# Performance work log

Hardware: AMD Instinct MI355X
Metric: run time of the kernel (lower is better)

Reference implementation:

```python
import jax, jax.numpy as jnp
import numpy as np

NUM_HEADS = 16
NEG_INF = -1e30


def setup_inputs() -> dict:
    key = jax.random.key(0)
    k1, k2, k3 = jax.random.split(key, 3)
    B, S, D = 2, 2048, 1024
    x = jax.random.normal(k1, (B, S, D), dtype=jnp.float32)
    # torch Linear(D, 3D, bias=False) stored here already transposed: y = x @ w_qkv
    w_qkv = jax.random.normal(k2, (D, 3 * D), dtype=jnp.float32) * 0.02
    w_out = jax.random.normal(k3, (D, D), dtype=jnp.float32) * 0.02
    return {"x": x, "w_qkv": w_qkv, "w_out": w_out}


def reference(x, w_qkv, w_out):
    B, S, D = x.shape
    H = NUM_HEADS
    dh = D // H
    qkv = x @ w_qkv                      # [B, S, 3D]
    q, k, v = jnp.split(qkv, 3, axis=-1)

    def to_heads(t):
        return t.reshape(B, S, H, dh).transpose(0, 2, 1, 3)  # [B, H, S, dh]

    q, k, v = to_heads(q), to_heads(k), to_heads(v)
    scale = jnp.asarray(dh, x.dtype) ** -0.5
    scores = jnp.einsum('bhqd,bhkd->bhqk', q, k) * scale     # [B, H, S, S]
    causal = jnp.tril(jnp.ones((S, S), dtype=bool))
    scores = jnp.where(causal, scores, NEG_INF)
    attn = jax.nn.softmax(scores, axis=-1)
    out = jnp.einsum('bhqk,bhkd->bhqd', attn, v)             # [B, H, S, dh]
    out = out.transpose(0, 2, 1, 3).reshape(B, S, D)
    return out @ w_out
```

## Files before the change

kernel.cpp:

```cpp
#include <hip/hip_runtime.h>

typedef unsigned short u16;
typedef unsigned int u32;

typedef __bf16 bf16x8 __attribute__((ext_vector_type(8)));
typedef _Float16 f16x8 __attribute__((ext_vector_type(8)));
typedef float f32x4 __attribute__((ext_vector_type(4)));

typedef __attribute__((address_space(1))) u32 as1_u32;
typedef __attribute__((address_space(3))) u32 as3_u32;

#define EKF 0.18033688011112042f

__device__ __forceinline__ u16 f2bf(float x) {
  u32 u = __float_as_uint(x);
  u = u + 0x7fffu + ((u >> 16) & 1u);
  return (u16)(u >> 16);
}
__device__ __forceinline__ u32 pack2(float a, float b) {
  return (u32)f2bf(a) | ((u32)f2bf(b) << 16);
}
__device__ __forceinline__ u32 pkf16(float a, float b) {
  return __builtin_bit_cast(u32, __builtin_amdgcn_cvt_pkrtz(a, b));
}
__device__ __forceinline__ u16 f2h(float a) {
  return (u16)(pkf16(a, a) & 0xffffu);
}
__device__ __forceinline__ void gld_lds16(const u16* g, const u16* l) {
  __builtin_amdgcn_global_load_lds((const as1_u32*)g, (as3_u32*)l, 16, 0, 0);
}

__global__ __launch_bounds__(256) void prepass_kernel(const float* __restrict__ x,
                                                      const float* __restrict__ w_qkv,
                                                      const float* __restrict__ w_out,
                                                      u16* __restrict__ xb,
                                                      u16* __restrict__ wqkvT,
                                                      u16* __restrict__ woutT) {
  __shared__ float tile[64][65];
  int bid = blockIdx.x;
  int t = threadIdx.x;
  if (bid < 4096) {
    int i = bid * 256 + t;
    float4 v = ((const float4*)x)[i];
    uint2 r;
    r.x = pack2(v.x, v.y);
    r.y = pack2(v.z, v.w);
    ((uint2*)xb)[i] = r;
    return;
  }
  const float* W;
  u16* WT;
  int K, N, bx, by;
  if (bid < 4096 + 768) {
    int b2 = bid - 4096;
    W = w_qkv; WT = wqkvT; K = 1024; N = 3072; bx = b2 & 15; by = b2 >> 4;
  } else {
    int b2 = bid - 4864;
    W = w_out; WT = woutT; K = 1024; N = 1024; bx = b2 & 15; by = b2 >> 4;
  }
  int k0 = bx * 64, n0 = by * 64;
  int r = t >> 4, c4 = (t & 15) * 4;
#pragma unroll
  for (int i = 0; i < 4; ++i) {
    int row = r + i * 16;
    float4 v = *(const float4*)&W[(size_t)(k0 + row) * N + n0 + c4];
    tile[row][c4 + 0] = v.x; tile[row][c4 + 1] = v.y;
    tile[row][c4 + 2] = v.z; tile[row][c4 + 3] = v.w;
  }
  __syncthreads();
#pragma unroll
  for (int i = 0; i < 4; ++i) {
    int n = r + i * 16;
    uint2 o;
    o.x = pack2(tile[c4 + 0][n], tile[c4 + 1][n]);
    o.y = pack2(tile[c4 + 2][n], tile[c4 + 3][n]);
    *(uint2*)&WT[(size_t)(n0 + n) * K + k0 + c4] = o;
  }
}

__global__ __launch_bounds__(512, 2) void gemm_qkv256_kernel(const u16* __restrict__ A,
                                                             const u16* __restrict__ BT,
                                                             u16* __restrict__ QK,
                                                             u16* __restrict__ VT) {
  __shared__ __attribute__((aligned(16))) u16 smem[65536];
  const int tid = threadIdx.x;
  const int wave = tid >> 6;
  const int lane = tid & 63;
  const int lr = lane & 15;
  const int kg = lane >> 4;
  const int l7 = lr & 7;
  const int wr = wave >> 2;
  const int wc = wave & 3;

  int b = blockIdx.x;
  int sw = (b & 7) * 24 + (b >> 3);
  const int bn = (sw % 12) * 256;
  const int bm = (sw / 12) * 256;

  const int srow = tid >> 3;
  const int scg = ((tid & 7) ^ (srow & 7)) * 8;
  const u16* pa = A + (size_t)(bm + srow) * 1024 + scg;
  const u16* pb = BT + (size_t)(bn + srow) * 1024 + scg;
  const u32 lw = (u32)wave * 512;

  f32x4 acc[8][4];
#pragma unroll
  for (int i = 0; i < 8; ++i)
#pragma unroll
    for (int j = 0; j < 4; ++j) {
      f32x4 z = {0.f, 0.f, 0.f, 0.f};
      acc[i][j] = z;
    }

  {
    u16* dA = (u16*)smem;
    u16* dB = (u16*)smem + 16384;
#pragma unroll
    for (int i = 0; i < 4; ++i) gld_lds16(pa + (size_t)(i * 64) * 1024, dA + lw + i * 4096);
#pragma unroll
    for (int i = 0; i < 4; ++i) gld_lds16(pb + (size_t)(i * 64) * 1024, dB + lw + i * 4096);
  }

  for (int t = 0; t < 16; ++t) {
    __syncthreads();
    const u16* bA = smem + (t & 1) * 32768;
    const u16* bB = bA + 16384;
    if (t + 1 < 16) {
      u16* dA = (u16*)smem + ((t + 1) & 1) * 32768;
      u16* dB = dA + 16384;
      const int k1 = (t + 1) * 64;
#pragma unroll
      for (int i = 0; i < 4; ++i) gld_lds16(pa + (size_t)(i * 64) * 1024 + k1, dA + lw + i * 4096);
#pragma unroll
      for (int i = 0; i < 4; ++i) gld_lds16(pb + (size_t)(i * 64) * 1024 + k1, dB + lw + i * 4096);
    }
    bf16x8 bfr[2][4];
#pragma unroll
    for (int kh = 0; kh < 2; ++kh)
#pragma unroll
      for (int ni = 0; ni < 4; ++ni)
        bfr[kh][ni] = *(const bf16x8*)(bB + (wc * 64 + ni * 16 + lr) * 64 +
                                       (((kh * 4 + kg) ^ l7) * 8));
#pragma unroll
    for (int ph = 0; ph < 4; ++ph) {
      const int mh = ph >> 1, kh = ph & 1;
      bf16x8 af[4];
#pragma unroll
      for (int mi = 0; mi < 4; ++mi)
        af[mi] = *(const bf16x8*)(bA + (wr * 128 + mh * 64 + mi * 16 + lr) * 64 +
                                  (((kh * 4 + kg) ^ l7) * 8));
      __builtin_amdgcn_s_barrier();
      __builtin_amdgcn_s_setprio(1);
#pragma unroll
      for (int mi = 0; mi < 4; ++mi)
#pragma unroll
        for (int ni = 0; ni < 4; ++ni)
          acc[mh * 4 + mi][ni] = __builtin_amdgcn_mfma_f32_16x16x32_bf16(
              bfr[kh][ni], af[mi], acc[mh * 4 + mi][ni], 0, 0, 0);
      __builtin_amdgcn_s_setprio(0);
      __builtin_amdgcn_s_barrier();
    }
  }

  __syncthreads();
  if (bn >= 2048) {
#pragma unroll
    for (int mi = 0; mi < 8; ++mi)
#pragma unroll
      for (int ni = 0; ni < 4; ++ni) {
        int r = bm + wr * 128 + mi * 16 + lr;
        int c = bn + wc * 64 + ni * 16 + kg * 4 - 2048;
        int bh2 = (r >> 11) * 16 + (c >> 6);
        int j = r & 2047;
        u16* vrow = VT + ((size_t)bh2 * 64 + (c & 63)) * 2048 + j;
        f32x4 a = acc[mi][ni];
#pragma unroll
        for (int rr = 0; rr < 4; ++rr) vrow[(size_t)rr * 2048] = f2h(a[rr]);
      }
  } else {
    float scale = (bn < 1024) ? EKF : 1.0f;
#pragma unroll
    for (int mi = 0; mi < 8; ++mi)
#pragma unroll
      for (int ni = 0; ni < 4; ++ni) {
        int row = wr * 128 + mi * 16 + lr;
        u32 off = (u32)row * 256 + wc * 64 + (((ni * 4 + kg) ^ (lr & 6)) * 4);
        f32x4 a = acc[mi][ni];
        *(uint2*)((u16*)smem + off) =
            make_uint2(pack2(a[0] * scale, a[1] * scale), pack2(a[2] * scale, a[3] * scale));
      }
    __syncthreads();
#pragma unroll
    for (int i = 0; i < 16; ++i) {
      int row = i * 16 + (tid >> 5);
      int lc = tid & 31;
      int blk = lc >> 3, cc = lc & 7;
      uint4 v = *(const uint4*)((const u16*)smem + (u32)row * 256 + blk * 64 +
                                (((2 * cc) ^ (row & 6)) * 4));
      *(uint4*)(QK + (size_t)(bm + row) * 2048 + bn + blk * 64 + cc * 8) = v;
    }
  }
}

__global__ __launch_bounds__(256, 2) void gemm_out_kernel(const u16* __restrict__ A,
                                                          const u16* __restrict__ BT,
                                                          float* __restrict__ C) {
  __shared__ __attribute__((aligned(16))) u16 smem[2][12288];
  const int tid = threadIdx.x;
  const int wave = tid >> 6;
  const int lane = tid & 63;
  const int lr = lane & 15;
  const int kg = lane >> 4;
  const int lr7 = lr & 7;
  const int wm = (wave >> 1) * 32;
  const int wn = (wave & 1) * 64;

  const int b = blockIdx.x;
  const int xcd = b & 7, loc = b >> 3;
  const int bm = (xcd * 8 + (loc >> 3)) * 64;
  const int bn = (loc & 7) * 128;

  const int sr = tid >> 3;
  const int scg = ((tid & 7) ^ (sr & 7)) * 8;
  const u16* pa = A + (size_t)(bm + sr) * 1024 + scg;
  const u16* pb = BT + (size_t)(bn + sr) * 1024 + scg;
  const u32 lw = (u32)wave * 512;

  f32x4 acc[2][4];
#pragma unroll
  for (int i = 0; i < 2; ++i)
#pragma unroll
    for (int j = 0; j < 4; ++j) {
      f32x4 z = {0.f, 0.f, 0.f, 0.f};
      acc[i][j] = z;
    }

  {
    u16* dA = smem[0];
    u16* dB = smem[0] + 4096;
#pragma unroll
    for (int i = 0; i < 2; ++i) gld_lds16(pa + (size_t)(i * 32) * 1024, dA + lw + i * 2048);
#pragma unroll
    for (int i = 0; i < 4; ++i) gld_lds16(pb + (size_t)(i * 32) * 1024, dB + lw + i * 2048);
  }

  for (int t = 0; t < 16; ++t) {
    __syncthreads();
    const u16* bA = smem[t & 1];
    const u16* bB = bA + 4096;
    if (t + 1 < 16) {
      u16* dA = smem[(t + 1) & 1];
      u16* dB = dA + 4096;
      const int k1 = (t + 1) * 64;
#pragma unroll
      for (int i = 0; i < 2; ++i) gld_lds16(pa + (size_t)(i * 32) * 1024 + k1, dA + lw + i * 2048);
#pragma unroll
      for (int i = 0; i < 4; ++i) gld_lds16(pb + (size_t)(i * 32) * 1024 + k1, dB + lw + i * 2048);
    }
#pragma unroll
    for (int kk = 0; kk < 2; ++kk) {
      const int ch = ((kk * 4 + kg) ^ lr7) * 8;
      bf16x8 af[2], bfr[4];
#pragma unroll
      for (int mi = 0; mi < 2; ++mi)
        af[mi] = *(const bf16x8*)(bA + (wm + mi * 16 + lr) * 64 + ch);
#pragma unroll
      for (int ni = 0; ni < 4; ++ni)
        bfr[ni] = *(const bf16x8*)(bB + (wn + ni * 16 + lr) * 64 + ch);
      __builtin_amdgcn_s_setprio(1);
#pragma unroll
      for (int mi = 0; mi < 2; ++mi)
#pragma unroll
        for (int ni = 0; ni < 4; ++ni)
          acc[mi][ni] = __builtin_amdgcn_mfma_f32_16x16x32_bf16(bfr[ni], af[mi], acc[mi][ni], 0, 0, 0);
      __builtin_amdgcn_s_setprio(0);
    }
  }

  float* buf = (float*)smem;
#pragma unroll
  for (int hc = 0; hc < 2; ++hc) {
    __syncthreads();
    if ((wave & 1) == hc) {
#pragma unroll
      for (int mi = 0; mi < 2; ++mi)
#pragma unroll
        for (int ni = 0; ni < 4; ++ni) {
          int row = wm + mi * 16 + lr;
          int cp = ((ni * 4 + kg) ^ lr) * 4;
          *(f32x4*)(buf + row * 64 + cp) = acc[mi][ni];
        }
    }
    __syncthreads();
#pragma unroll
    for (int i = 0; i < 4; ++i) {
      int row = i * 16 + (tid >> 4);
      int lc = tid & 15;
      float4 v = *(const float4*)(buf + row * 64 + ((lc ^ (row & 15)) * 4));
      *(float4*)(C + (size_t)(bm + row) * 1024 + bn + hc * 64 + lc * 4) = v;
    }
  }
}

__global__ __launch_bounds__(256, 4) void attn_mfma_kernel(const u16* __restrict__ qk,
                                                           const u16* __restrict__ vt,
                                                           u16* __restrict__ out) {
  __shared__ __attribute__((aligned(16))) u16 sK[2][64 * 64];
  __shared__ __attribute__((aligned(16))) u16 sV[2][64 * 64];
  __shared__ __attribute__((aligned(16))) u16 sP[4][16 * 64];

  const int tid = threadIdx.x;
  const int wave = tid >> 6;
  const int lane = tid & 63;
  const int lr = lane & 15;
  const int kg = lane >> 4;
  const int l7 = lr & 7;

  int idx = blockIdx.x;
  int qi = 31 - (idx >> 5);
  int bh = (idx & 7) * 4 + ((idx >> 3) & 3);
  int b = bh >> 4, h = bh & 15;
  int q0 = qi * 64;

  const u16* qbase = qk + (size_t)b * 2048 * 2048 + h * 64;
  const u16* kbase = qbase + 1024;
  const u16* vbase = vt + (size_t)bh * 64 * 2048;
  u16* obase = out + (size_t)b * 2048 * 1024 + h * 64;

  const int sra = wave * 16 + (lane >> 3);
  const int srb = sra + 8;
  const int sc = lane & 7;
  const u32 koffA = (u32)sra * 2048 + (u32)((sc ^ (sra & 7)) * 8);
  const u32 koffB = (u32)srb * 2048 + (u32)((sc ^ (srb & 7)) * 8);
  const u32 ldsA = (wave * 2 + 0) * 512;
  const u32 ldsB = (wave * 2 + 1) * 512;

  const int qcol = q0 + wave * 16 + lr;
  bf16x8 qf0, qf1;
  {
    const u16* qrow = qbase + (size_t)qcol * 2048;
    qf0 = *(const bf16x8*)(qrow + kg * 8);
    qf1 = *(const bf16x8*)(qrow + 32 + kg * 8);
  }

  const u32 ka0 = (u32)(lr * 64 + ((kg ^ l7) * 8));
  const u32 ka1 = (u32)(lr * 64 + (((4 + kg) ^ l7) * 8));
  u16* const sPw = sP[wave];
  const u32 pr0 = (u32)(lr * 64 + (((kg * 2) ^ (l7 << 1)) * 4));
  const u32 pr1 = (u32)(lr * 64 + (((8 + kg * 2) ^ (l7 << 1)) * 4));

  f32x4 oacc[4];
#pragma unroll
  for (int i = 0; i < 4; ++i) {
    f32x4 z = {0.f, 0.f, 0.f, 0.f};
    oacc[i] = z;
  }
  float lsum = 0.f;

  const int nrounds = qi + 1;
  gld_lds16(kbase + koffA, sK[0] + ldsA);
  gld_lds16(kbase + koffB, sK[0] + ldsB);
  gld_lds16(vbase + koffA, sV[0] + ldsA);
  gld_lds16(vbase + koffB, sV[0] + ldsB);
  __syncthreads();

  for (int t = 0; t < nrounds; ++t) {
    if (t + 1 < nrounds) {
      int j1 = (t + 1) * 64;
      u16* dK = sK[(t + 1) & 1];
      u16* dV = sV[(t + 1) & 1];
      gld_lds16(kbase + (size_t)j1 * 2048 + koffA, dK + ldsA);
      gld_lds16(kbase + (size_t)j1 * 2048 + koffB, dK + ldsB);
      gld_lds16(vbase + j1 + koffA, dV + ldsA);
      gld_lds16(vbase + j1 + koffB, dV + ldsB);
    }
    const u16* sKb = sK[t & 1];
    const u16* sVb = sV[t & 1];
    const bool diag = (t == qi);

#pragma unroll
    for (int jt = 0; jt < 4; ++jt) {
      u16* pw = sPw + lr * 64 + (((jt * 4 + kg) ^ (l7 << 1)) * 4);
      if (!diag || jt <= wave) {
        bf16x8 kf0 = *(const bf16x8*)(sKb + jt * 1024 + ka0);
        bf16x8 kf1 = *(const bf16x8*)(sKb + jt * 1024 + ka1);
        f32x4 c = {0.f, 0.f, 0.f, 0.f};
        c = __builtin_amdgcn_mfma_f32_16x16x32_bf16(kf0, qf0, c, 0, 0, 0);
        c = __builtin_amdgcn_mfma_f32_16x16x32_bf16(kf1, qf1, c, 0, 0, 0);
        float p0 = exp2f(c[0]);
        float p1 = exp2f(c[1]);
        float p2 = exp2f(c[2]);
        float p3 = exp2f(c[3]);
        if (diag && jt == wave) {
          int jr = kg * 4;
          p0 = (jr + 0 <= lr) ? p0 : 0.f;
          p1 = (jr + 1 <= lr) ? p1 : 0.f;
          p2 = (jr + 2 <= lr) ? p2 : 0.f;
          p3 = (jr + 3 <= lr) ? p3 : 0.f;
        }
        lsum += (p0 + p1) + (p2 + p3);
        *(uint2*)pw = make_uint2(pkf16(p0, p1), pkf16(p2, p3));
      } else {
        *(uint2*)pw = make_uint2(0u, 0u);
      }
    }

    asm volatile("" ::: "memory");

    f16x8 pf0 = *(const f16x8*)(sPw + pr0);
    f16x8 pf1 = *(const f16x8*)(sPw + pr1);
    __builtin_amdgcn_s_setprio(1);
#pragma unroll
    for (int dt = 0; dt < 4; ++dt) {
      f16x8 vf0 = *(const f16x8*)(sVb + dt * 1024 + ka0);
      f16x8 vf1 = *(const f16x8*)(sVb + dt * 1024 + ka1);
      oacc[dt] = __builtin_amdgcn_mfma_f32_16x16x32_f16(vf0, pf0, oacc[dt], 0, 0, 0);
      oacc[dt] = __builtin_amdgcn_mfma_f32_16x16x32_f16(vf1, pf1, oacc[dt], 0, 0, 0);
    }
    __builtin_amdgcn_s_setprio(0);
    __syncthreads();
  }

  lsum += __shfl_xor(lsum, 16);
  lsum += __shfl_xor(lsum, 32);
  float inv = 1.0f / lsum;

  u16* orow = obase + (size_t)qcol * 1024;
#pragma unroll
  for (int dt = 0; dt < 4; ++dt) {
    uint2 o2 = make_uint2(pack2(oacc[dt][0] * inv, oacc[dt][1] * inv),
                          pack2(oacc[dt][2] * inv, oacc[dt][3] * inv));
    *(uint2*)(orow + dt * 16 + kg * 4) = o2;
  }
}

extern "C" void kernel_launch(void* const* d_in, const int* in_sizes, int n_in,
                              void* d_out, int out_size, void* d_ws, size_t ws_size,
                              hipStream_t stream) {
  const float* x = (const float*)d_in[0];
  const float* w_qkv = (const float*)d_in[1];
  const float* w_out = (const float*)d_in[2];
  float* out = (float*)d_out;

  char* ws = (char*)d_ws;
  u16* xb    = (u16*)(ws);
  u16* wqkvT = (u16*)(ws + (8u << 20));
  u16* woutT = (u16*)(ws + (14u << 20));
  u16* qkb   = (u16*)(ws + (16u << 20));
  u16* vtb   = (u16*)(ws + (32u << 20));
  u16* attn  = (u16*)(ws + (40u << 20));

  prepass_kernel<<<5120, 256, 0, stream>>>(x, w_qkv, w_out, xb, wqkvT, woutT);

  gemm_qkv256_kernel<<<192, 512, 0, stream>>>(xb, wqkvT, qkb, vtb);

  attn_mfma_kernel<<<1024, 256, 0, stream>>>(qkb, vtb, attn);

  gemm_out_kernel<<<512, 256, 0, stream>>>(attn, woutT, out);
}
```

Measured before the change: 163.1 us.

## Split attention waves into 2x2 query/key grid with LDS partial-sum reduction

Changes the wave decomposition in the attention kernel. Each wave used to own 16 query rows across all 64 keys; now each wave owns 32 query rows and 32 keys. Each K and V fragment loaded from LDS is therefore reused across two query subtiles, which roughly halves LDS fragment reads per MFMA. The cost is a final cross-wave reduction of partial outputs and row sums through shared memory, plus an extra barrier and more accumulator registers.

```diff
diff --git a/kernel.cpp b/kernel.cpp
--- a/kernel.cpp
+++ b/kernel.cpp
@@ -307,7 +307,7 @@
                                                            u16* __restrict__ out) {
   __shared__ __attribute__((aligned(16))) u16 sK[2][64 * 64];
   __shared__ __attribute__((aligned(16))) u16 sV[2][64 * 64];
-  __shared__ __attribute__((aligned(16))) u16 sP[4][16 * 64];
+  __shared__ __attribute__((aligned(16))) u16 sP[4][32 * 32];
 
   const int tid = threadIdx.x;
   const int wave = tid >> 6;
@@ -315,6 +315,8 @@
   const int lr = lane & 15;
   const int kg = lane >> 4;
   const int l7 = lr & 7;
+  const int qh = wave & 1;
+  const int jh = wave >> 1;
 
   int idx = blockIdx.x;
   int qi = 31 - (idx >> 5);
@@ -335,27 +337,30 @@
   const u32 ldsA = (wave * 2 + 0) * 512;
   const u32 ldsB = (wave * 2 + 1) * 512;
 
-  const int qcol = q0 + wave * 16 + lr;
-  bf16x8 qf0, qf1;
-  {
-    const u16* qrow = qbase + (size_t)qcol * 2048;
-    qf0 = *(const bf16x8*)(qrow + kg * 8);
-    qf1 = *(const bf16x8*)(qrow + 32 + kg * 8);
+  bf16x8 qf[2][2];
+#pragma unroll
+  for (int qs = 0; qs < 2; ++qs) {
+    const u16* qrow = qbase + (size_t)(q0 + qh * 32 + qs * 16 + lr) * 2048;
+    qf[qs][0] = *(const bf16x8*)(qrow + kg * 8);
+    qf[qs][1] = *(const bf16x8*)(qrow + 32 + kg * 8);
   }
 
   const u32 ka0 = (u32)(lr * 64 + ((kg ^ l7) * 8));
   const u32 ka1 = (u32)(lr * 64 + (((4 + kg) ^ l7) * 8));
+  const u32 kav = jh ? ka1 : ka0;
   u16* const sPw = sP[wave];
-  const u32 pr0 = (u32)(lr * 64 + (((kg * 2) ^ (l7 << 1)) * 4));
-  const u32 pr1 = (u32)(lr * 64 + (((8 + kg * 2) ^ (l7 << 1)) * 4));
-
-  f32x4 oacc[4];
-#pragma unroll
-  for (int i = 0; i < 4; ++i) {
-    f32x4 z = {0.f, 0.f, 0.f, 0.f};
-    oacc[i] = z;
-  }
-  float lsum = 0.f;
+  const u32 pkey = (u32)((lr & 3) << 1);
+  const u32 prd = (u32)(((2 * kg) ^ pkey) * 4);
+
+  f32x4 oacc[2][4];
+#pragma unroll
+  for (int qs = 0; qs < 2; ++qs)
+#pragma unroll
+    for (int dt = 0; dt < 4; ++dt) {
+      f32x4 z = {0.f, 0.f, 0.f, 0.f};
+      oacc[qs][dt] = z;
+    }
+  float ls[2] = {0.f, 0.f};
 
   const int nrounds = qi + 1;
   gld_lds16(kbase + koffA, sK[0] + ldsA);
@@ -379,58 +384,86 @@
     const bool diag = (t == qi);
 
 #pragma unroll
-    for (int jt = 0; jt < 4; ++jt) {
-      u16* pw = sPw + lr * 64 + (((jt * 4 + kg) ^ (l7 << 1)) * 4);
-      if (!diag || jt <= wave) {
-        bf16x8 kf0 = *(const bf16x8*)(sKb + jt * 1024 + ka0);
-        bf16x8 kf1 = *(const bf16x8*)(sKb + jt * 1024 + ka1);
-        f32x4 c = {0.f, 0.f, 0.f, 0.f};
-        c = __builtin_amdgcn_mfma_f32_16x16x32_bf16(kf0, qf0, c, 0, 0, 0);
-        c = __builtin_amdgcn_mfma_f32_16x16x32_bf16(kf1, qf1, c, 0, 0, 0);
-        float p0 = exp2f(c[0]);
-        float p1 = exp2f(c[1]);
-        float p2 = exp2f(c[2]);
-        float p3 = exp2f(c[3]);
-        if (diag && jt == wave) {
-          int jr = kg * 4;
-          p0 = (jr + 0 <= lr) ? p0 : 0.f;
-          p1 = (jr + 1 <= lr) ? p1 : 0.f;
-          p2 = (jr + 2 <= lr) ? p2 : 0.f;
-          p3 = (jr + 3 <= lr) ? p3 : 0.f;
+    for (int jtl = 0; jtl < 2; ++jtl) {
+      const int jtg = jh * 2 + jtl;
+      bf16x8 kf0 = *(const bf16x8*)(sKb + jtg * 1024 + ka0);
+      bf16x8 kf1 = *(const bf16x8*)(sKb + jtg * 1024 + ka1);
+#pragma unroll
+      for (int qs = 0; qs < 2; ++qs) {
+        const int qmin = qh * 32 + qs * 16;
+        u16* pw = sPw + (qs * 16 + lr) * 32 + (((jtl * 4 + kg) ^ pkey) * 4);
+        if (!diag || jtg * 16 <= qmin + 15) {
+          f32x4 c = {0.f, 0.f, 0.f, 0.f};
+          c = __builtin_amdgcn_mfma_f32_16x16x32_bf16(kf0, qf[qs][0], c, 0, 0, 0);
+          c = __builtin_amdgcn_mfma_f32_16x16x32_bf16(kf1, qf[qs][1], c, 0, 0, 0);
+          float p0 = exp2f(c[0]);
+          float p1 = exp2f(c[1]);
+          float p2 = exp2f(c[2]);
+          float p3 = exp2f(c[3]);
+          if (diag && jtg * 16 + 15 > qmin) {
+            int jr = jtg * 16 + kg * 4 - qmin;
+            p0 = (jr + 0 <= lr) ? p0 : 0.f;
+            p1 = (jr + 1 <= lr) ? p1 : 0.f;
+            p2 = (jr + 2 <= lr) ? p2 : 0.f;
+            p3 = (jr + 3 <= lr) ? p3 : 0.f;
+          }
+          ls[qs] += (p0 + p1) + (p2 + p3);
+          *(uint2*)pw = make_uint2(pkf16(p0, p1), pkf16(p2, p3));
+        } else {
+          *(uint2*)pw = make_uint2(0u, 0u);
         }
-        lsum += (p0 + p1) + (p2 + p3);
-        *(uint2*)pw = make_uint2(pkf16(p0, p1), pkf16(p2, p3));
-      } else {
-        *(uint2*)pw = make_uint2(0u, 0u);
       }
     }
 
     asm volatile("" ::: "memory");
 
-    f16x8 pf0 = *(const f16x8*)(sPw + pr0);
-    f16x8 pf1 = *(const f16x8*)(sPw + pr1);
+    f16x8 pf0 = *(const f16x8*)(sPw + (0 * 16 + lr) * 32 + prd);
+    f16x8 pf1 = *(const f16x8*)(sPw + (1 * 16 + lr) * 32 + prd);
     __builtin_amdgcn_s_setprio(1);
 #pragma unroll
     for (int dt = 0; dt < 4; ++dt) {
-      f16x8 vf0 = *(const f16x8*)(sVb + dt * 1024 + ka0);
-      f16x8 vf1 = *(const f16x8*)(sVb + dt * 1024 + ka1);
-      oacc[dt] = __builtin_amdgcn_mfma_f32_16x16x32_f16(vf0, pf0, oacc[dt], 0, 0, 0);
-      oacc[dt] = __builtin_amdgcn_mfma_f32_16x16x32_f16(vf1, pf1, oacc[dt], 0, 0, 0);
+      f16x8 vf = *(const f16x8*)(sVb + dt * 1024 + kav);
+      oacc[0][dt] = __builtin_amdgcn_mfma_f32_16x16x32_f16(vf, pf0, oacc[0][dt], 0, 0, 0);
+      oacc[1][dt] = __builtin_amdgcn_mfma_f32_16x16x32_f16(vf, pf1, oacc[1][dt], 0, 0, 0);
     }
     __builtin_amdgcn_s_setprio(0);
     __syncthreads();
   }
 
-  lsum += __shfl_xor(lsum, 16);
-  lsum += __shfl_xor(lsum, 32);
-  float inv = 1.0f / lsum;
-
-  u16* orow = obase + (size_t)qcol * 1024;
-#pragma unroll
-  for (int dt = 0; dt < 4; ++dt) {
-    uint2 o2 = make_uint2(pack2(oacc[dt][0] * inv, oacc[dt][1] * inv),
-                          pack2(oacc[dt][2] * inv, oacc[dt][3] * inv));
-    *(uint2*)(orow + dt * 16 + kg * 4) = o2;
+  ls[0] += __shfl_xor(ls[0], 16);
+  ls[0] += __shfl_xor(ls[0], 32);
+  ls[1] += __shfl_xor(ls[1], 16);
+  ls[1] += __shfl_xor(ls[1], 32);
+
+  float* obuf = (float*)sK;
+  float* lbuf = (float*)sV;
+  if (jh == 1) {
+#pragma unroll
+    for (int qs = 0; qs < 2; ++qs) {
+      int q = qh * 32 + qs * 16 + lr;
+#pragma unroll
+      for (int dt = 0; dt < 4; ++dt)
+        *(f32x4*)(obuf + q * 64 + (((dt * 4 + kg) ^ l7) * 4)) = oacc[qs][dt];
+      if (kg == 0) lbuf[q] = ls[qs];
+    }
+  }
+  __syncthreads();
+  if (jh == 0) {
+#pragma unroll
+    for (int qs = 0; qs < 2; ++qs) {
+      int q = qh * 32 + qs * 16 + lr;
+      float inv = 1.0f / (ls[qs] + lbuf[q]);
+      u16* orow = obase + (size_t)(q0 + q) * 1024;
+#pragma unroll
+      for (int dt = 0; dt < 4; ++dt) {
+        f32x4 po = *(const f32x4*)(obuf + q * 64 + (((dt * 4 + kg) ^ l7) * 4));
+        float o0 = (oacc[qs][dt][0] + po[0]) * inv;
+        float o1 = (oacc[qs][dt][1] + po[1]) * inv;
+        float o2 = (oacc[qs][dt][2] + po[2]) * inv;
+        float o3 = (oacc[qs][dt][3] + po[3]) * inv;
+        *(uint2*)(orow + dt * 16 + kg * 4) = make_uint2(pack2(o0, o1), pack2(o2, o3));
+      }
+    }
   }
 }
 
```

Result: no change. 165.6 us (+1.5%).

## Switch attention to 32x32 MFMA with register-resident P via permlane swap

Applied to the files above, without the earlier changes.

Reworks the attention inner loop to use 32x32x16 MFMA tiles: waves split queries into two 32-row halves and keys into two 32-column halves. Probabilities are repacked in registers with v_permlane32_swap instead of round-tripping through shared memory, so the sP buffer goes away. Partial outputs and row sums from the two key halves are combined through LDS at the end. This trades fewer LDS writes/reads and fewer MFMA issues for an extra final reduction and coarser causal masking, since the diagonal tile now computes masked work across whole 32-wide blocks.

```diff
diff --git a/kernel.cpp b/kernel.cpp
--- a/kernel.cpp
+++ b/kernel.cpp
@@ -6,6 +6,8 @@
 typedef __bf16 bf16x8 __attribute__((ext_vector_type(8)));
 typedef _Float16 f16x8 __attribute__((ext_vector_type(8)));
 typedef float f32x4 __attribute__((ext_vector_type(4)));
+typedef float f32x16 __attribute__((ext_vector_type(16)));
+typedef u32 u32x4 __attribute__((ext_vector_type(4)));
 
 typedef __attribute__((address_space(1))) u32 as1_u32;
 typedef __attribute__((address_space(3))) u32 as3_u32;
@@ -307,14 +309,14 @@
                                                            u16* __restrict__ out) {
   __shared__ __attribute__((aligned(16))) u16 sK[2][64 * 64];
   __shared__ __attribute__((aligned(16))) u16 sV[2][64 * 64];
-  __shared__ __attribute__((aligned(16))) u16 sP[4][16 * 64];
 
   const int tid = threadIdx.x;
   const int wave = tid >> 6;
   const int lane = tid & 63;
-  const int lr = lane & 15;
-  const int kg = lane >> 4;
-  const int l7 = lr & 7;
+  const int l31 = lane & 31;
+  const int hi = lane >> 5;
+  const int qh = wave & 1;
+  const int jh = wave >> 1;
 
   int idx = blockIdx.x;
   int qi = 31 - (idx >> 5);
@@ -335,27 +337,18 @@
   const u32 ldsA = (wave * 2 + 0) * 512;
   const u32 ldsB = (wave * 2 + 1) * 512;
 
-  const int qcol = q0 + wave * 16 + lr;
-  bf16x8 qf0, qf1;
+  const int qcol = q0 + qh * 32 + l31;
+  bf16x8 qf[4];
   {
     const u16* qrow = qbase + (size_t)qcol * 2048;
-    qf0 = *(const bf16x8*)(qrow + kg * 8);
-    qf1 = *(const bf16x8*)(qrow + 32 + kg * 8);
-  }
-
-  const u32 ka0 = (u32)(lr * 64 + ((kg ^ l7) * 8));
-  const u32 ka1 = (u32)(lr * 64 + (((4 + kg) ^ l7) * 8));
-  u16* const sPw = sP[wave];
-  const u32 pr0 = (u32)(lr * 64 + (((kg * 2) ^ (l7 << 1)) * 4));
-  const u32 pr1 = (u32)(lr * 64 + (((8 + kg * 2) ^ (l7 << 1)) * 4));
-
-  f32x4 oacc[4];
-#pragma unroll
-  for (int i = 0; i < 4; ++i) {
-    f32x4 z = {0.f, 0.f, 0.f, 0.f};
-    oacc[i] = z;
-  }
-  float lsum = 0.f;
+#pragma unroll
+    for (int s = 0; s < 4; ++s) qf[s] = *(const bf16x8*)(qrow + s * 16 + hi * 8);
+  }
+
+  f32x16 oacc[2];
+#pragma unroll
+  for (int i = 0; i < 16; ++i) { oacc[0][i] = 0.f; oacc[1][i] = 0.f; }
+  float ls = 0.f;
 
   const int nrounds = qi + 1;
   gld_lds16(kbase + koffA, sK[0] + ldsA);
@@ -378,59 +371,92 @@
     const u16* sVb = sV[t & 1];
     const bool diag = (t == qi);
 
-#pragma unroll
-    for (int jt = 0; jt < 4; ++jt) {
-      u16* pw = sPw + lr * 64 + (((jt * 4 + kg) ^ (l7 << 1)) * 4);
-      if (!diag || jt <= wave) {
-        bf16x8 kf0 = *(const bf16x8*)(sKb + jt * 1024 + ka0);
-        bf16x8 kf1 = *(const bf16x8*)(sKb + jt * 1024 + ka1);
-        f32x4 c = {0.f, 0.f, 0.f, 0.f};
-        c = __builtin_amdgcn_mfma_f32_16x16x32_bf16(kf0, qf0, c, 0, 0, 0);
-        c = __builtin_amdgcn_mfma_f32_16x16x32_bf16(kf1, qf1, c, 0, 0, 0);
-        float p0 = exp2f(c[0]);
-        float p1 = exp2f(c[1]);
-        float p2 = exp2f(c[2]);
-        float p3 = exp2f(c[3]);
-        if (diag && jt == wave) {
-          int jr = kg * 4;
-          p0 = (jr + 0 <= lr) ? p0 : 0.f;
-          p1 = (jr + 1 <= lr) ? p1 : 0.f;
-          p2 = (jr + 2 <= lr) ? p2 : 0.f;
-          p3 = (jr + 3 <= lr) ? p3 : 0.f;
-        }
-        lsum += (p0 + p1) + (p2 + p3);
-        *(uint2*)pw = make_uint2(pkf16(p0, p1), pkf16(p2, p3));
-      } else {
-        *(uint2*)pw = make_uint2(0u, 0u);
+    f32x16 c;
+#pragma unroll
+    for (int i = 0; i < 16; ++i) c[i] = 0.f;
+#pragma unroll
+    for (int s = 0; s < 4; ++s) {
+      const u32 row = (u32)(jh * 32 + l31);
+      bf16x8 kf = *(const bf16x8*)(sKb + row * 64 + (((2 * s + hi) ^ (row & 7)) * 8));
+      c = __builtin_amdgcn_mfma_f32_32x32x16_bf16(kf, qf[s], c, 0, 0, 0);
+    }
+    float p[16];
+    const int qrel = qh * 32 + l31;
+#pragma unroll
+    for (int r = 0; r < 16; ++r) {
+      int joff = jh * 32 + (r & 3) + 8 * (r >> 2) + 4 * hi;
+      float e = exp2f(c[r]);
+      p[r] = (!diag || (joff <= qrel)) ? e : 0.f;
+    }
+    {
+      float s0 = (p[0] + p[1]) + (p[2] + p[3]);
+      float s1 = (p[4] + p[5]) + (p[6] + p[7]);
+      float s2 = (p[8] + p[9]) + (p[10] + p[11]);
+      float s3 = (p[12] + p[13]) + (p[14] + p[15]);
+      ls += (s0 + s1) + (s2 + s3);
+    }
+    u32 c01 = pkf16(p[0], p[1]),   c23 = pkf16(p[2], p[3]);
+    u32 c45 = pkf16(p[4], p[5]),   c67 = pkf16(p[6], p[7]);
+    u32 c89 = pkf16(p[8], p[9]),   cab = pkf16(p[10], p[11]);
+    u32 ccd = pkf16(p[12], p[13]), cef = pkf16(p[14], p[15]);
+    asm volatile("v_permlane32_swap_b32 %0, %1" : "+v"(c01), "+v"(c45));
+    asm volatile("v_permlane32_swap_b32 %0, %1" : "+v"(c23), "+v"(c67));
+    asm volatile("v_permlane32_swap_b32 %0, %1" : "+v"(c89), "+v"(ccd));
+    asm volatile("v_permlane32_swap_b32 %0, %1" : "+v"(cab), "+v"(cef));
+    u32x4 w0 = {c01, c23, c45, c67};
+    u32x4 w1 = {c89, cab, ccd, cef};
+    f16x8 pa0 = __builtin_bit_cast(f16x8, w0);
+    f16x8 pa1 = __builtin_bit_cast(f16x8, w1);
+
+    __builtin_amdgcn_s_setprio(1);
+#pragma unroll
+    for (int dh = 0; dh < 2; ++dh) {
+      const u32 row = (u32)(dh * 32 + l31);
+#pragma unroll
+      for (int s2 = 0; s2 < 2; ++s2) {
+        f16x8 vf = *(const f16x8*)(sVb + row * 64 +
+                                   (((4 * jh + 2 * s2 + hi) ^ (row & 7)) * 8));
+        oacc[dh] = __builtin_amdgcn_mfma_f32_32x32x16_f16(
+            vf, (s2 == 0) ? pa0 : pa1, oacc[dh], 0, 0, 0);
       }
     }
-
-    asm volatile("" ::: "memory");
-
-    f16x8 pf0 = *(const f16x8*)(sPw + pr0);
-    f16x8 pf1 = *(const f16x8*)(sPw + pr1);
-    __builtin_amdgcn_s_setprio(1);
-#pragma unroll
-    for (int dt = 0; dt < 4; ++dt) {
-      f16x8 vf0 = *(const f16x8*)(sVb + dt * 1024 + ka0);
-      f16x8 vf1 = *(const f16x8*)(sVb + dt * 1024 + ka1);
-      oacc[dt] = __builtin_amdgcn_mfma_f32_16x16x32_f16(vf0, pf0, oacc[dt], 0, 0, 0);
-      oacc[dt] = __builtin_amdgcn_mfma_f32_16x16x32_f16(vf1, pf1, oacc[dt], 0, 0, 0);
-    }
     __builtin_amdgcn_s_setprio(0);
     __syncthreads();
   }
 
-  lsum += __shfl_xor(lsum, 16);
-  lsum += __shfl_xor(lsum, 32);
-  float inv = 1.0f / lsum;
-
-  u16* orow = obase + (size_t)qcol * 1024;
-#pragma unroll
-  for (int dt = 0; dt < 4; ++dt) {
-    uint2 o2 = make_uint2(pack2(oacc[dt][0] * inv, oacc[dt][1] * inv),
-                          pack2(oacc[dt][2] * inv, oacc[dt][3] * inv));
-    *(uint2*)(orow + dt * 16 + kg * 4) = o2;
+  ls += __shfl_xor(ls, 32);
+
+  float* obuf = (float*)sK;
+  float* lbuf = (float*)sV;
+  const int q = qh * 32 + l31;
+  if (jh == 1) {
+#pragma unroll
+    for (int dh = 0; dh < 2; ++dh)
+#pragma unroll
+      for (int g = 0; g < 4; ++g) {
+        int ch = dh * 8 + g * 2 + hi;
+        f32x4 w = {oacc[dh][4 * g + 0], oacc[dh][4 * g + 1],
+                   oacc[dh][4 * g + 2], oacc[dh][4 * g + 3]};
+        *(f32x4*)(obuf + q * 64 + ((ch ^ (q & 15)) * 4)) = w;
+      }
+    if (hi == 0) lbuf[q] = ls;
+  }
+  __syncthreads();
+  if (jh == 0) {
+    float inv = 1.0f / (ls + lbuf[q]);
+    u16* orow = obase + (size_t)qcol * 1024;
+#pragma unroll
+    for (int dh = 0; dh < 2; ++dh)
+#pragma unroll
+      for (int g = 0; g < 4; ++g) {
+        int ch = dh * 8 + g * 2 + hi;
+        f32x4 po = *(const f32x4*)(obuf + q * 64 + ((ch ^ (q & 15)) * 4));
+        float o0 = (oacc[dh][4 * g + 0] + po[0]) * inv;
+        float o1 = (oacc[dh][4 * g + 1] + po[1]) * inv;
+        float o2 = (oacc[dh][4 * g + 2] + po[2]) * inv;
+        float o3 = (oacc[dh][4 * g + 3] + po[3]) * inv;
+        *(uint2*)(orow + dh * 32 + g * 8 + hi * 4) = make_uint2(pack2(o0, o1), pack2(o2, o3));
+      }
   }
 }
 
```

After: 162.5 us. About the same (-0.4%).
